# Performance work log

Hardware: AMD Instinct MI355X
Metric: run time of the kernel (lower is better)

Reference implementation:

```python
import jax, jax.numpy as jnp
import numpy as np

CLIP = 5.0
LATENT, HIDDEN, INPUT, OUT = 64, 128, 128, 32


def setup_inputs() -> dict:
    key = jax.random.key(0)
    ks = jax.random.split(key, 9)
    B, T = 256, 1024
    inp = {
        "input_sequence": jax.random.normal(ks[0], (B, T, INPUT), jnp.float32),
        "A": jax.random.uniform(ks[1], (LATENT,), jnp.float32, -0.1, 0.1),
        "W1": jax.random.normal(ks[2], (LATENT, HIDDEN), jnp.float32) * (1.0 / np.sqrt(HIDDEN)),
        "W2": jax.random.normal(ks[3], (HIDDEN, LATENT), jnp.float32) * (1.0 / np.sqrt(LATENT)),
        "h1": jnp.zeros((LATENT,), jnp.float32),
        "h2": jnp.zeros((HIDDEN,), jnp.float32),
        "C": jax.random.normal(ks[4], (LATENT, INPUT), jnp.float32) * (1.0 / np.sqrt(INPUT)),
        "Wout": jax.random.normal(ks[5], (OUT, LATENT), jnp.float32) * (1.0 / np.sqrt(LATENT)),
        "bout": jnp.zeros((OUT,), jnp.float32),
    }
    return inp


def reference(input_sequence, A, W1, W2, h1, h2, C, Wout, bout):
    # Precompute input drive C @ s_t for all timesteps: [B, T, L]
    drive = jnp.einsum('bti,li->btl', input_sequence, C)
    B = input_sequence.shape[0]
    z0 = jnp.zeros((B, A.shape[0]), input_sequence.dtype)

    def step(z, u):
        # z: [B, L], u: [B, L] (C @ s_t)
        hidden = jax.nn.relu(z @ W2.T + h2)               # [B, H]
        z_next = z * A + hidden @ W1.T + h1 + u           # [B, L]
        z_next = jnp.clip(z_next, -CLIP, CLIP)
        return z_next, None

    zT, _ = jax.lax.scan(step, z0, jnp.swapaxes(drive, 0, 1))  # scan over T
    return zT @ Wout.T + bout                                   # [B, OUT]
```

## Files before the change

kernel.cpp:

```cpp
#include <hip/hip_runtime.h>
#include <hip/hip_bf16.h>

#define BATCH 256
#define TSTEPS 1024
#define NIN 128
#define NL 64
#define NH 128
#define NOUT 32

typedef __attribute__((ext_vector_type(8))) short short8;
typedef __attribute__((ext_vector_type(4))) float f32x4;

__device__ inline int pk2(float x, float y) {
    __hip_bfloat162 h = __float22bfloat162_rn(make_float2(x, y));
    union { __hip_bfloat162 h; int i; } u;
    u.h = h;
    return u.i;
}
__device__ inline short bf1(float x) {
    __hip_bfloat16 h = __float2bfloat16(x);
    union { __hip_bfloat16 h; short s; } u;
    u.h = h;
    return u.s;
}

#define WG_BARRIER() asm volatile("s_waitcnt lgkmcnt(0)\n\ts_barrier" ::: "memory")

__launch_bounds__(256, 1)
__global__ void ugemm_mfma(const float* __restrict__ input,
                           const float* __restrict__ C,
                           const float* __restrict__ h1,
                           unsigned short* __restrict__ u16) {
    const int lane = threadIdx.x & 63;
    const int wv   = threadIdx.x >> 6;
    const int c = lane & 15;
    const int q = lane >> 4;
    const long wbase = ((long)blockIdx.x * 4 + wv) * 128;

    short8 cA[4][4];
    #pragma unroll
    for (int mt = 0; mt < 4; ++mt)
        #pragma unroll
        for (int kf = 0; kf < 4; ++kf) {
            const float* p = C + (mt * 16 + c) * NIN + kf * 32 + q * 8;
            float4 r0 = *(const float4*)p;
            float4 r1 = *(const float4*)(p + 4);
            union { short8 s; int i[4]; } f;
            f.i[0] = pk2(r0.x, r0.y); f.i[1] = pk2(r0.z, r0.w);
            f.i[2] = pk2(r1.x, r1.y); f.i[3] = pk2(r1.z, r1.w);
            cA[mt][kf] = f.s;
        }
    f32x4 h1f[4];
    #pragma unroll
    for (int mt = 0; mt < 4; ++mt)
        h1f[mt] = *(const f32x4*)(h1 + mt * 16 + q * 4);

    float4 raw[8], rawn[8];
    {
        const float* sr = input + (wbase + c) * NIN;
        #pragma unroll
        for (int kf = 0; kf < 4; ++kf) {
            raw[2*kf]   = *(const float4*)(sr + kf * 32 + q * 8);
            raw[2*kf+1] = *(const float4*)(sr + kf * 32 + q * 8 + 4);
        }
    }

    for (int it = 0; it < 8; ++it) {
        if (it < 7) {
            const float* sr = input + (wbase + (it + 1) * 16 + c) * NIN;
            #pragma unroll
            for (int kf = 0; kf < 4; ++kf) {
                rawn[2*kf]   = *(const float4*)(sr + kf * 32 + q * 8);
                rawn[2*kf+1] = *(const float4*)(sr + kf * 32 + q * 8 + 4);
            }
        }
        short8 bf[4];
        #pragma unroll
        for (int kf = 0; kf < 4; ++kf) {
            union { short8 s; int i[4]; } f;
            f.i[0] = pk2(raw[2*kf].x,   raw[2*kf].y);
            f.i[1] = pk2(raw[2*kf].z,   raw[2*kf].w);
            f.i[2] = pk2(raw[2*kf+1].x, raw[2*kf+1].y);
            f.i[3] = pk2(raw[2*kf+1].z, raw[2*kf+1].w);
            bf[kf] = f.s;
        }
        long rr = wbase + it * 16 + c;
        int b = (int)(rr >> 10), t = (int)(rr & 1023);
        unsigned short* ubase = u16 + ((size_t)t * 256 + b) * 64 + q * 4;
        #pragma unroll
        for (int mt = 0; mt < 4; ++mt) {
            f32x4 acc = __builtin_amdgcn_mfma_f32_16x16x32_bf16(cA[mt][0], bf[0], h1f[mt], 0, 0, 0);
            acc = __builtin_amdgcn_mfma_f32_16x16x32_bf16(cA[mt][1], bf[1], acc, 0, 0, 0);
            acc = __builtin_amdgcn_mfma_f32_16x16x32_bf16(cA[mt][2], bf[2], acc, 0, 0, 0);
            acc = __builtin_amdgcn_mfma_f32_16x16x32_bf16(cA[mt][3], bf[3], acc, 0, 0, 0);
            *(int2*)(ubase + mt * 16) =
                make_int2(pk2(acc[0], acc[1]), pk2(acc[2], acc[3]));
        }
        #pragma unroll
        for (int j = 0; j < 8; ++j) raw[j] = rawn[j];
    }
}

__launch_bounds__(256, 1)
__global__ void plrnn_scan_mfma(const float* __restrict__ A,
                                const float* __restrict__ W1,
                                const float* __restrict__ W2,
                                const float* __restrict__ h2,
                                const unsigned short* __restrict__ u16,
                                const float* __restrict__ Wout,
                                const float* __restrict__ bout,
                                float* __restrict__ out) {
    __shared__ __attribute__((aligned(16))) unsigned short zbuf[16 * 72];
    __shared__ __attribute__((aligned(16))) unsigned short hbuf[16 * 136];

    const int lane = threadIdx.x & 63;
    const int w    = threadIdx.x >> 6;
    const int c = lane & 15;
    const int q = lane >> 4;
    const int bbase = blockIdx.x * 16;

    short8 aw2[2][2];
    #pragma unroll
    for (int i = 0; i < 2; ++i)
        #pragma unroll
        for (int kt = 0; kt < 2; ++kt) {
            const float* p = W2 + ((2*w + i) * 16 + c) * NL + kt * 32 + q * 8;
            short8 f;
            #pragma unroll
            for (int j = 0; j < 8; ++j) f[j] = bf1(p[j]);
            aw2[i][kt] = f;
        }
    short8 aw1[4];
    #pragma unroll
    for (int kt = 0; kt < 4; ++kt) {
        const float* p = W1 + (w * 16 + c) * NH + kt * 32 + q * 8;
        short8 f;
        #pragma unroll
        for (int j = 0; j < 8; ++j) f[j] = bf1(p[j]);
        aw1[kt] = f;
    }
    f32x4 h2f[2];
    #pragma unroll
    for (int i = 0; i < 2; ++i)
        h2f[i] = *(const f32x4*)(h2 + (2*w + i) * 16 + q * 4);
    const f32x4 af = *(const f32x4*)(A + w * 16 + q * 4);

    f32x4 zf = {0.f, 0.f, 0.f, 0.f};

    const unsigned short* ub = u16 + ((size_t)(bbase + c)) * 64 + w * 16 + q * 4;
    int2 ucur = *(const int2*)ub;
    int2 unx  = *(const int2*)(ub + 16384);

    for (int t = 0; t < TSTEPS; ++t) {
        *(int2*)&zbuf[c * 72 + w * 16 + q * 4] =
            make_int2(pk2(zf[0], zf[1]), pk2(zf[2], zf[3]));
        WG_BARRIER();
        short8 bz0 = *(short8*)&zbuf[c * 72 + q * 8];
        short8 bz1 = *(short8*)&zbuf[c * 72 + 32 + q * 8];

        int tp = (t + 2 < TSTEPS) ? t + 2 : TSTEPS - 1;
        int2 upf = *(const int2*)(ub + (size_t)tp * 16384);

        #pragma unroll
        for (int i = 0; i < 2; ++i) {
            f32x4 acc = __builtin_amdgcn_mfma_f32_16x16x32_bf16(aw2[i][0], bz0, h2f[i], 0, 0, 0);
            acc = __builtin_amdgcn_mfma_f32_16x16x32_bf16(aw2[i][1], bz1, acc, 0, 0, 0);
            *(int2*)&hbuf[c * 136 + (2*w + i) * 16 + q * 4] =
                make_int2(pk2(fmaxf(acc[0], 0.f), fmaxf(acc[1], 0.f)),
                          pk2(fmaxf(acc[2], 0.f), fmaxf(acc[3], 0.f)));
        }
        WG_BARRIER();
        short8 bh0 = *(short8*)&hbuf[c * 136 + q * 8];
        short8 bh1 = *(short8*)&hbuf[c * 136 + 32 + q * 8];
        short8 bh2 = *(short8*)&hbuf[c * 136 + 64 + q * 8];
        short8 bh3 = *(short8*)&hbuf[c * 136 + 96 + q * 8];

        f32x4 cin;
        cin[0] = fmaf(zf[0], af[0], __int_as_float(ucur.x << 16));
        cin[1] = fmaf(zf[1], af[1], __int_as_float(ucur.x & 0xffff0000));
        cin[2] = fmaf(zf[2], af[2], __int_as_float(ucur.y << 16));
        cin[3] = fmaf(zf[3], af[3], __int_as_float(ucur.y & 0xffff0000));
        f32x4 acc = __builtin_amdgcn_mfma_f32_16x16x32_bf16(aw1[0], bh0, cin, 0, 0, 0);
        acc = __builtin_amdgcn_mfma_f32_16x16x32_bf16(aw1[1], bh1, acc, 0, 0, 0);
        acc = __builtin_amdgcn_mfma_f32_16x16x32_bf16(aw1[2], bh2, acc, 0, 0, 0);
        acc = __builtin_amdgcn_mfma_f32_16x16x32_bf16(aw1[3], bh3, acc, 0, 0, 0);
        #pragma unroll
        for (int e = 0; e < 4; ++e)
            zf[e] = fminf(fmaxf(acc[e], -5.f), 5.f);
        ucur = unx;
        unx  = upf;
    }

    *(int2*)&zbuf[c * 72 + w * 16 + q * 4] =
        make_int2(pk2(zf[0], zf[1]), pk2(zf[2], zf[3]));
    WG_BARRIER();
    if (w < 2) {
        short8 fz0 = *(short8*)&zbuf[c * 72 + q * 8];
        short8 fz1 = *(short8*)&zbuf[c * 72 + 32 + q * 8];
        const float* p0 = Wout + (w * 16 + c) * NL + q * 8;
        const float* p1 = p0 + 32;
        short8 fa, fb;
        #pragma unroll
        for (int j = 0; j < 8; ++j) { fa[j] = bf1(p0[j]); fb[j] = bf1(p1[j]); }
        f32x4 cb = *(const f32x4*)(bout + w * 16 + q * 4);
        f32x4 acc = __builtin_amdgcn_mfma_f32_16x16x32_bf16(fa, fz0, cb, 0, 0, 0);
        acc = __builtin_amdgcn_mfma_f32_16x16x32_bf16(fb, fz1, acc, 0, 0, 0);
        *(f32x4*)&out[(bbase + c) * 32 + w * 16 + q * 4] = acc;
    }
}

extern "C" void kernel_launch(void* const* d_in, const int* in_sizes, int n_in,
                              void* d_out, int out_size, void* d_ws, size_t ws_size,
                              hipStream_t stream) {
    const float* input = (const float*)d_in[0];
    const float* A     = (const float*)d_in[1];
    const float* W1    = (const float*)d_in[2];
    const float* W2    = (const float*)d_in[3];
    const float* h1    = (const float*)d_in[4];
    const float* h2    = (const float*)d_in[5];
    const float* C     = (const float*)d_in[6];
    const float* Wout  = (const float*)d_in[7];
    const float* bout  = (const float*)d_in[8];
    float* out = (float*)d_out;

    unsigned short* u16 = (unsigned short*)d_ws;

    ugemm_mfma<<<dim3(512), dim3(256), 0, stream>>>(input, C, h1, u16);
    plrnn_scan_mfma<<<dim3(16), dim3(256), 0, stream>>>(
        A, W1, W2, h2, u16, Wout, bout, out);
}
```

Measured before the change: 517.8 us.

## Run recurrent scan in a single wavefront per batch tile, removing barriers

The scan kernel is restructured so one 64-lane wavefront per 16-batch tile does all the per-step matmuls, instead of four waves that synchronised twice per timestep with workgroup barriers. LDS exchanges now rely only on a compiler fence because a single wave runs in lockstep. The time loop is also unrolled by two with ping-pong prefetch buffers, and clamping uses fmed3. Each wave now issues four times as many serially dependent MFMAs per step and holds more weights in registers, trading barrier latency for longer per-wave compute chains.

```diff
diff --git a/kernel.cpp b/kernel.cpp
--- a/kernel.cpp
+++ b/kernel.cpp
@@ -24,7 +24,7 @@
     return u.s;
 }
 
-#define WG_BARRIER() asm volatile("s_waitcnt lgkmcnt(0)\n\ts_barrier" ::: "memory")
+#define KFENCE() asm volatile("" ::: "memory")
 
 __launch_bounds__(256, 1)
 __global__ void ugemm_mfma(const float* __restrict__ input,
@@ -101,8 +101,8 @@
     }
 }
 
-__launch_bounds__(256, 1)
-__global__ void plrnn_scan_mfma(const float* __restrict__ A,
+__launch_bounds__(64, 1)
+__global__ void plrnn_scan_wave(const float* __restrict__ A,
                                 const float* __restrict__ W1,
                                 const float* __restrict__ W2,
                                 const float* __restrict__ h2,
@@ -110,102 +110,167 @@
                                 const float* __restrict__ Wout,
                                 const float* __restrict__ bout,
                                 float* __restrict__ out) {
-    __shared__ __attribute__((aligned(16))) unsigned short zbuf[16 * 72];
-    __shared__ __attribute__((aligned(16))) unsigned short hbuf[16 * 136];
+    __shared__ __attribute__((aligned(16))) unsigned short zs[16 * 72];
+    __shared__ __attribute__((aligned(16))) unsigned short hs[16 * 136];
 
     const int lane = threadIdx.x & 63;
-    const int w    = threadIdx.x >> 6;
     const int c = lane & 15;
     const int q = lane >> 4;
     const int bbase = blockIdx.x * 16;
 
-    short8 aw2[2][2];
-    #pragma unroll
-    for (int i = 0; i < 2; ++i)
+    short8 aw2[8][2];
+    #pragma unroll
+    for (int mt = 0; mt < 8; ++mt)
         #pragma unroll
         for (int kt = 0; kt < 2; ++kt) {
-            const float* p = W2 + ((2*w + i) * 16 + c) * NL + kt * 32 + q * 8;
+            const float* p = W2 + (mt * 16 + c) * NL + kt * 32 + q * 8;
             short8 f;
             #pragma unroll
             for (int j = 0; j < 8; ++j) f[j] = bf1(p[j]);
-            aw2[i][kt] = f;
-        }
-    short8 aw1[4];
-    #pragma unroll
-    for (int kt = 0; kt < 4; ++kt) {
-        const float* p = W1 + (w * 16 + c) * NH + kt * 32 + q * 8;
-        short8 f;
-        #pragma unroll
-        for (int j = 0; j < 8; ++j) f[j] = bf1(p[j]);
-        aw1[kt] = f;
-    }
-    f32x4 h2f[2];
-    #pragma unroll
-    for (int i = 0; i < 2; ++i)
-        h2f[i] = *(const f32x4*)(h2 + (2*w + i) * 16 + q * 4);
-    const f32x4 af = *(const f32x4*)(A + w * 16 + q * 4);
-
-    f32x4 zf = {0.f, 0.f, 0.f, 0.f};
-
-    const unsigned short* ub = u16 + ((size_t)(bbase + c)) * 64 + w * 16 + q * 4;
-    int2 ucur = *(const int2*)ub;
-    int2 unx  = *(const int2*)(ub + 16384);
-
-    for (int t = 0; t < TSTEPS; ++t) {
-        *(int2*)&zbuf[c * 72 + w * 16 + q * 4] =
-            make_int2(pk2(zf[0], zf[1]), pk2(zf[2], zf[3]));
-        WG_BARRIER();
-        short8 bz0 = *(short8*)&zbuf[c * 72 + q * 8];
-        short8 bz1 = *(short8*)&zbuf[c * 72 + 32 + q * 8];
-
-        int tp = (t + 2 < TSTEPS) ? t + 2 : TSTEPS - 1;
-        int2 upf = *(const int2*)(ub + (size_t)tp * 16384);
-
-        #pragma unroll
-        for (int i = 0; i < 2; ++i) {
-            f32x4 acc = __builtin_amdgcn_mfma_f32_16x16x32_bf16(aw2[i][0], bz0, h2f[i], 0, 0, 0);
-            acc = __builtin_amdgcn_mfma_f32_16x16x32_bf16(aw2[i][1], bz1, acc, 0, 0, 0);
-            *(int2*)&hbuf[c * 136 + (2*w + i) * 16 + q * 4] =
-                make_int2(pk2(fmaxf(acc[0], 0.f), fmaxf(acc[1], 0.f)),
-                          pk2(fmaxf(acc[2], 0.f), fmaxf(acc[3], 0.f)));
-        }
-        WG_BARRIER();
-        short8 bh0 = *(short8*)&hbuf[c * 136 + q * 8];
-        short8 bh1 = *(short8*)&hbuf[c * 136 + 32 + q * 8];
-        short8 bh2 = *(short8*)&hbuf[c * 136 + 64 + q * 8];
-        short8 bh3 = *(short8*)&hbuf[c * 136 + 96 + q * 8];
-
-        f32x4 cin;
-        cin[0] = fmaf(zf[0], af[0], __int_as_float(ucur.x << 16));
-        cin[1] = fmaf(zf[1], af[1], __int_as_float(ucur.x & 0xffff0000));
-        cin[2] = fmaf(zf[2], af[2], __int_as_float(ucur.y << 16));
-        cin[3] = fmaf(zf[3], af[3], __int_as_float(ucur.y & 0xffff0000));
-        f32x4 acc = __builtin_amdgcn_mfma_f32_16x16x32_bf16(aw1[0], bh0, cin, 0, 0, 0);
-        acc = __builtin_amdgcn_mfma_f32_16x16x32_bf16(aw1[1], bh1, acc, 0, 0, 0);
-        acc = __builtin_amdgcn_mfma_f32_16x16x32_bf16(aw1[2], bh2, acc, 0, 0, 0);
-        acc = __builtin_amdgcn_mfma_f32_16x16x32_bf16(aw1[3], bh3, acc, 0, 0, 0);
-        #pragma unroll
-        for (int e = 0; e < 4; ++e)
-            zf[e] = fminf(fmaxf(acc[e], -5.f), 5.f);
-        ucur = unx;
-        unx  = upf;
-    }
-
-    *(int2*)&zbuf[c * 72 + w * 16 + q * 4] =
-        make_int2(pk2(zf[0], zf[1]), pk2(zf[2], zf[3]));
-    WG_BARRIER();
-    if (w < 2) {
-        short8 fz0 = *(short8*)&zbuf[c * 72 + q * 8];
-        short8 fz1 = *(short8*)&zbuf[c * 72 + 32 + q * 8];
-        const float* p0 = Wout + (w * 16 + c) * NL + q * 8;
-        const float* p1 = p0 + 32;
-        short8 fa, fb;
-        #pragma unroll
-        for (int j = 0; j < 8; ++j) { fa[j] = bf1(p0[j]); fb[j] = bf1(p1[j]); }
-        f32x4 cb = *(const f32x4*)(bout + w * 16 + q * 4);
-        f32x4 acc = __builtin_amdgcn_mfma_f32_16x16x32_bf16(fa, fz0, cb, 0, 0, 0);
-        acc = __builtin_amdgcn_mfma_f32_16x16x32_bf16(fb, fz1, acc, 0, 0, 0);
-        *(f32x4*)&out[(bbase + c) * 32 + w * 16 + q * 4] = acc;
+            aw2[mt][kt] = f;
+        }
+    short8 aw1[4][4];
+    #pragma unroll
+    for (int lt = 0; lt < 4; ++lt)
+        #pragma unroll
+        for (int kt = 0; kt < 4; ++kt) {
+            const float* p = W1 + (lt * 16 + c) * NH + kt * 32 + q * 8;
+            short8 f;
+            #pragma unroll
+            for (int j = 0; j < 8; ++j) f[j] = bf1(p[j]);
+            aw1[lt][kt] = f;
+        }
+    f32x4 h2f[8];
+    #pragma unroll
+    for (int mt = 0; mt < 8; ++mt)
+        h2f[mt] = *(const f32x4*)(h2 + mt * 16 + q * 4);
+    f32x4 af[4];
+    #pragma unroll
+    for (int lt = 0; lt < 4; ++lt)
+        af[lt] = *(const f32x4*)(A + lt * 16 + q * 4);
+
+    const unsigned short* ub = u16 + (size_t)(bbase + c) * 64 + q * 4;
+    int2 uP[4], uQ[4];
+    #pragma unroll
+    for (int lt = 0; lt < 4; ++lt) {
+        uP[lt] = *(const int2*)(ub + lt * 16);
+        uQ[lt] = *(const int2*)(ub + 16384 + lt * 16);
+    }
+
+    f32x4 zf[4];
+    #pragma unroll
+    for (int lt = 0; lt < 4; ++lt) zf[lt] = (f32x4){0.f, 0.f, 0.f, 0.f};
+
+    short8 bz0 = (short8){0, 0, 0, 0, 0, 0, 0, 0};
+    short8 bz1 = (short8){0, 0, 0, 0, 0, 0, 0, 0};
+
+    f32x4 cin[4];
+    #pragma unroll
+    for (int lt = 0; lt < 4; ++lt) {
+        cin[lt][0] = __int_as_float(uP[lt].x << 16);
+        cin[lt][1] = __int_as_float(uP[lt].x & 0xffff0000);
+        cin[lt][2] = __int_as_float(uP[lt].y << 16);
+        cin[lt][3] = __int_as_float(uP[lt].y & 0xffff0000);
+    }
+
+    auto step = [&](int2 (&pf)[4], const int2 (&tail)[4], const int T) {
+        f32x4 ha[4];
+        #pragma unroll
+        for (int mt = 0; mt < 4; ++mt)
+            ha[mt] = __builtin_amdgcn_mfma_f32_16x16x32_bf16(aw2[mt][0], bz0, h2f[mt], 0, 0, 0);
+        #pragma unroll
+        for (int mt = 0; mt < 4; ++mt)
+            ha[mt] = __builtin_amdgcn_mfma_f32_16x16x32_bf16(aw2[mt][1], bz1, ha[mt], 0, 0, 0);
+        #pragma unroll
+        for (int mt = 0; mt < 4; ++mt)
+            *(int2*)&hs[c * 136 + mt * 16 + q * 4] = make_int2(
+                pk2(fmaxf(ha[mt][0], 0.f), fmaxf(ha[mt][1], 0.f)),
+                pk2(fmaxf(ha[mt][2], 0.f), fmaxf(ha[mt][3], 0.f)));
+        KFENCE();
+        short8 bh0 = *(short8*)&hs[c * 136 + q * 8];
+        short8 bh1 = *(short8*)&hs[c * 136 + 32 + q * 8];
+
+        f32x4 hb[4];
+        #pragma unroll
+        for (int mt = 0; mt < 4; ++mt)
+            hb[mt] = __builtin_amdgcn_mfma_f32_16x16x32_bf16(aw2[mt + 4][0], bz0, h2f[mt + 4], 0, 0, 0);
+        #pragma unroll
+        for (int mt = 0; mt < 4; ++mt)
+            hb[mt] = __builtin_amdgcn_mfma_f32_16x16x32_bf16(aw2[mt + 4][1], bz1, hb[mt], 0, 0, 0);
+        #pragma unroll
+        for (int mt = 0; mt < 4; ++mt)
+            *(int2*)&hs[c * 136 + (mt + 4) * 16 + q * 4] = make_int2(
+                pk2(fmaxf(hb[mt][0], 0.f), fmaxf(hb[mt][1], 0.f)),
+                pk2(fmaxf(hb[mt][2], 0.f), fmaxf(hb[mt][3], 0.f)));
+        KFENCE();
+        short8 bh2 = *(short8*)&hs[c * 136 + 64 + q * 8];
+        short8 bh3 = *(short8*)&hs[c * 136 + 96 + q * 8];
+
+        const int tp = (T + 2 < TSTEPS) ? T + 2 : TSTEPS - 1;
+        #pragma unroll
+        for (int lt = 0; lt < 4; ++lt)
+            pf[lt] = *(const int2*)(ub + (size_t)tp * 16384 + lt * 16);
+
+        f32x4 za[4];
+        #pragma unroll
+        for (int lt = 0; lt < 4; ++lt)
+            za[lt] = __builtin_amdgcn_mfma_f32_16x16x32_bf16(aw1[lt][0], bh0, cin[lt], 0, 0, 0);
+        #pragma unroll
+        for (int lt = 0; lt < 4; ++lt)
+            za[lt] = __builtin_amdgcn_mfma_f32_16x16x32_bf16(aw1[lt][1], bh1, za[lt], 0, 0, 0);
+        #pragma unroll
+        for (int lt = 0; lt < 4; ++lt)
+            za[lt] = __builtin_amdgcn_mfma_f32_16x16x32_bf16(aw1[lt][2], bh2, za[lt], 0, 0, 0);
+        #pragma unroll
+        for (int lt = 0; lt < 4; ++lt)
+            za[lt] = __builtin_amdgcn_mfma_f32_16x16x32_bf16(aw1[lt][3], bh3, za[lt], 0, 0, 0);
+
+        #pragma unroll
+        for (int lt = 0; lt < 4; ++lt) {
+            zf[lt][0] = __builtin_amdgcn_fmed3f(za[lt][0], -5.f, 5.f);
+            zf[lt][1] = __builtin_amdgcn_fmed3f(za[lt][1], -5.f, 5.f);
+            zf[lt][2] = __builtin_amdgcn_fmed3f(za[lt][2], -5.f, 5.f);
+            zf[lt][3] = __builtin_amdgcn_fmed3f(za[lt][3], -5.f, 5.f);
+        }
+        #pragma unroll
+        for (int lt = 0; lt < 4; ++lt)
+            *(int2*)&zs[c * 72 + lt * 16 + q * 4] =
+                make_int2(pk2(zf[lt][0], zf[lt][1]), pk2(zf[lt][2], zf[lt][3]));
+        KFENCE();
+        bz0 = *(short8*)&zs[c * 72 + q * 8];
+        bz1 = *(short8*)&zs[c * 72 + 32 + q * 8];
+
+        #pragma unroll
+        for (int lt = 0; lt < 4; ++lt) {
+            cin[lt][0] = fmaf(zf[lt][0], af[lt][0], __int_as_float(tail[lt].x << 16));
+            cin[lt][1] = fmaf(zf[lt][1], af[lt][1], __int_as_float(tail[lt].x & 0xffff0000));
+            cin[lt][2] = fmaf(zf[lt][2], af[lt][2], __int_as_float(tail[lt].y << 16));
+            cin[lt][3] = fmaf(zf[lt][3], af[lt][3], __int_as_float(tail[lt].y & 0xffff0000));
+        }
+    };
+
+    for (int t = 0; t < TSTEPS; t += 2) {
+        step(uP, uQ, t);
+        step(uQ, uP, t + 1);
+    }
+
+    short8 wo[2][2];
+    #pragma unroll
+    for (int ot = 0; ot < 2; ++ot)
+        #pragma unroll
+        for (int kt = 0; kt < 2; ++kt) {
+            const float* p = Wout + (ot * 16 + c) * NL + kt * 32 + q * 8;
+            short8 f;
+            #pragma unroll
+            for (int j = 0; j < 8; ++j) f[j] = bf1(p[j]);
+            wo[ot][kt] = f;
+        }
+    #pragma unroll
+    for (int ot = 0; ot < 2; ++ot) {
+        f32x4 ob = *(const f32x4*)(bout + ot * 16 + q * 4);
+        f32x4 acc = __builtin_amdgcn_mfma_f32_16x16x32_bf16(wo[ot][0], bz0, ob, 0, 0, 0);
+        acc = __builtin_amdgcn_mfma_f32_16x16x32_bf16(wo[ot][1], bz1, acc, 0, 0, 0);
+        *(f32x4*)&out[(size_t)(bbase + c) * 32 + ot * 16 + q * 4] = acc;
     }
 }
 
@@ -226,6 +291,6 @@
     unsigned short* u16 = (unsigned short*)d_ws;
 
     ugemm_mfma<<<dim3(512), dim3(256), 0, stream>>>(input, C, h1, u16);
-    plrnn_scan_mfma<<<dim3(16), dim3(256), 0, stream>>>(
+    plrnn_scan_wave<<<dim3(16), dim3(64), 0, stream>>>(
         A, W1, W2, h2, u16, Wout, bout, out);
 }
```

Result: slower. 835.7 us (+61.4%).

## Split-K the W1 GEMM across waves and rebuild fragments with permlane swaps

Applied to the files above, without the earlier changes.

The recurrent scan kernel now has each wave own a K-slice of the hidden dimension for the W1 product. Each wave computes partial sums for all latent tiles, and the partials are reduced through a double-buffered LDS buffer. The B fragments for h and z are built in registers with permlane32/permlane16 swaps instead of round-tripping through LDS. This drops one workgroup barrier per timestep, trading it for extra MFMAs, more LDS traffic for the partials, and redundant reduction work in every wave.

```diff
diff --git a/kernel.cpp b/kernel.cpp
--- a/kernel.cpp
+++ b/kernel.cpp
@@ -10,6 +10,7 @@
 
 typedef __attribute__((ext_vector_type(8))) short short8;
 typedef __attribute__((ext_vector_type(4))) float f32x4;
+typedef __attribute__((ext_vector_type(2))) unsigned int u32x2;
 
 __device__ inline int pk2(float x, float y) {
     __hip_bfloat162 h = __float22bfloat162_rn(make_float2(x, y));
@@ -25,6 +26,19 @@
 }
 
 #define WG_BARRIER() asm volatile("s_waitcnt lgkmcnt(0)\n\ts_barrier" ::: "memory")
+
+__device__ inline short8 mk_bfrag(int a0, int a1, int b0, int b1) {
+    u32x2 s0 = __builtin_amdgcn_permlane32_swap((unsigned)a0, (unsigned)b0, false, false);
+    u32x2 t0 = __builtin_amdgcn_permlane16_swap(s0[0], s0[1], false, false);
+    u32x2 s1 = __builtin_amdgcn_permlane32_swap((unsigned)a1, (unsigned)b1, false, false);
+    u32x2 t1 = __builtin_amdgcn_permlane16_swap(s1[0], s1[1], false, false);
+    union { int i[4]; short8 s; } u;
+    u.i[0] = (int)t0[0];
+    u.i[1] = (int)t1[0];
+    u.i[2] = (int)t0[1];
+    u.i[3] = (int)t1[1];
+    return u.s;
+}
 
 __launch_bounds__(256, 1)
 __global__ void ugemm_mfma(const float* __restrict__ input,
@@ -102,16 +116,15 @@
 }
 
 __launch_bounds__(256, 1)
-__global__ void plrnn_scan_mfma(const float* __restrict__ A,
-                                const float* __restrict__ W1,
-                                const float* __restrict__ W2,
-                                const float* __restrict__ h2,
-                                const unsigned short* __restrict__ u16,
-                                const float* __restrict__ Wout,
-                                const float* __restrict__ bout,
-                                float* __restrict__ out) {
-    __shared__ __attribute__((aligned(16))) unsigned short zbuf[16 * 72];
-    __shared__ __attribute__((aligned(16))) unsigned short hbuf[16 * 136];
+__global__ void plrnn_scan_ks(const float* __restrict__ A,
+                              const float* __restrict__ W1,
+                              const float* __restrict__ W2,
+                              const float* __restrict__ h2,
+                              const unsigned short* __restrict__ u16,
+                              const float* __restrict__ Wout,
+                              const float* __restrict__ bout,
+                              float* __restrict__ out) {
+    __shared__ __attribute__((aligned(16))) float pbuf[2][4][4][64][4];
 
     const int lane = threadIdx.x & 63;
     const int w    = threadIdx.x >> 6;
@@ -124,7 +137,7 @@
     for (int i = 0; i < 2; ++i)
         #pragma unroll
         for (int kt = 0; kt < 2; ++kt) {
-            const float* p = W2 + ((2*w + i) * 16 + c) * NL + kt * 32 + q * 8;
+            const float* p = W2 + ((2 * w + i) * 16 + c) * NL + kt * 32 + q * 8;
             short8 f;
             #pragma unroll
             for (int j = 0; j < 8; ++j) f[j] = bf1(p[j]);
@@ -132,80 +145,116 @@
         }
     short8 aw1[4];
     #pragma unroll
-    for (int kt = 0; kt < 4; ++kt) {
-        const float* p = W1 + (w * 16 + c) * NH + kt * 32 + q * 8;
+    for (int lt = 0; lt < 4; ++lt) {
+        const float* p = W1 + (lt * 16 + c) * NH + w * 32 + q * 8;
         short8 f;
         #pragma unroll
         for (int j = 0; j < 8; ++j) f[j] = bf1(p[j]);
-        aw1[kt] = f;
+        aw1[lt] = f;
     }
     f32x4 h2f[2];
     #pragma unroll
     for (int i = 0; i < 2; ++i)
-        h2f[i] = *(const f32x4*)(h2 + (2*w + i) * 16 + q * 4);
+        h2f[i] = *(const f32x4*)(h2 + (2 * w + i) * 16 + q * 4);
     const f32x4 af = *(const f32x4*)(A + w * 16 + q * 4);
 
-    f32x4 zf = {0.f, 0.f, 0.f, 0.f};
-
-    const unsigned short* ub = u16 + ((size_t)(bbase + c)) * 64 + w * 16 + q * 4;
-    int2 ucur = *(const int2*)ub;
-    int2 unx  = *(const int2*)(ub + 16384);
-
-    for (int t = 0; t < TSTEPS; ++t) {
-        *(int2*)&zbuf[c * 72 + w * 16 + q * 4] =
-            make_int2(pk2(zf[0], zf[1]), pk2(zf[2], zf[3]));
+    const unsigned short* ub = u16 + (size_t)(bbase + c) * 64 + w * 16 + q * 4;
+    int2 uP = *(const int2*)ub;
+    int2 uQ = *(const int2*)(ub + 16384);
+
+    short8 bz0 = (short8){0, 0, 0, 0, 0, 0, 0, 0};
+    short8 bz1 = (short8){0, 0, 0, 0, 0, 0, 0, 0};
+    f32x4 cin;
+    cin[0] = __int_as_float(uP.x << 16);
+    cin[1] = __int_as_float(uP.x & 0xffff0000);
+    cin[2] = __int_as_float(uP.y << 16);
+    cin[3] = __int_as_float(uP.y & 0xffff0000);
+    const f32x4 zero4 = {0.f, 0.f, 0.f, 0.f};
+
+    auto step = [&](int2& pf, const int2& tail, const int T, const int buf) {
+        f32x4 ha[2];
+        #pragma unroll
+        for (int i = 0; i < 2; ++i)
+            ha[i] = __builtin_amdgcn_mfma_f32_16x16x32_bf16(aw2[i][0], bz0, h2f[i], 0, 0, 0);
+        #pragma unroll
+        for (int i = 0; i < 2; ++i)
+            ha[i] = __builtin_amdgcn_mfma_f32_16x16x32_bf16(aw2[i][1], bz1, ha[i], 0, 0, 0);
+
+        int hp[2][2];
+        #pragma unroll
+        for (int i = 0; i < 2; ++i) {
+            hp[i][0] = pk2(fmaxf(ha[i][0], 0.f), fmaxf(ha[i][1], 0.f));
+            hp[i][1] = pk2(fmaxf(ha[i][2], 0.f), fmaxf(ha[i][3], 0.f));
+        }
+        short8 bh = mk_bfrag(hp[0][0], hp[0][1], hp[1][0], hp[1][1]);
+
+        f32x4 za[4];
+        #pragma unroll
+        for (int lt = 0; lt < 4; ++lt)
+            za[lt] = __builtin_amdgcn_mfma_f32_16x16x32_bf16(
+                aw1[lt], bh, (lt == w) ? cin : zero4, 0, 0, 0);
+
+        #pragma unroll
+        for (int lt = 0; lt < 4; ++lt)
+            *(f32x4*)&pbuf[buf][w][lt][lane][0] = za[lt];
+
         WG_BARRIER();
-        short8 bz0 = *(short8*)&zbuf[c * 72 + q * 8];
-        short8 bz1 = *(short8*)&zbuf[c * 72 + 32 + q * 8];
-
-        int tp = (t + 2 < TSTEPS) ? t + 2 : TSTEPS - 1;
-        int2 upf = *(const int2*)(ub + (size_t)tp * 16384);
-
-        #pragma unroll
-        for (int i = 0; i < 2; ++i) {
-            f32x4 acc = __builtin_amdgcn_mfma_f32_16x16x32_bf16(aw2[i][0], bz0, h2f[i], 0, 0, 0);
-            acc = __builtin_amdgcn_mfma_f32_16x16x32_bf16(aw2[i][1], bz1, acc, 0, 0, 0);
-            *(int2*)&hbuf[c * 136 + (2*w + i) * 16 + q * 4] =
-                make_int2(pk2(fmaxf(acc[0], 0.f), fmaxf(acc[1], 0.f)),
-                          pk2(fmaxf(acc[2], 0.f), fmaxf(acc[3], 0.f)));
-        }
-        WG_BARRIER();
-        short8 bh0 = *(short8*)&hbuf[c * 136 + q * 8];
-        short8 bh1 = *(short8*)&hbuf[c * 136 + 32 + q * 8];
-        short8 bh2 = *(short8*)&hbuf[c * 136 + 64 + q * 8];
-        short8 bh3 = *(short8*)&hbuf[c * 136 + 96 + q * 8];
-
-        f32x4 cin;
-        cin[0] = fmaf(zf[0], af[0], __int_as_float(ucur.x << 16));
-        cin[1] = fmaf(zf[1], af[1], __int_as_float(ucur.x & 0xffff0000));
-        cin[2] = fmaf(zf[2], af[2], __int_as_float(ucur.y << 16));
-        cin[3] = fmaf(zf[3], af[3], __int_as_float(ucur.y & 0xffff0000));
-        f32x4 acc = __builtin_amdgcn_mfma_f32_16x16x32_bf16(aw1[0], bh0, cin, 0, 0, 0);
-        acc = __builtin_amdgcn_mfma_f32_16x16x32_bf16(aw1[1], bh1, acc, 0, 0, 0);
-        acc = __builtin_amdgcn_mfma_f32_16x16x32_bf16(aw1[2], bh2, acc, 0, 0, 0);
-        acc = __builtin_amdgcn_mfma_f32_16x16x32_bf16(aw1[3], bh3, acc, 0, 0, 0);
-        #pragma unroll
-        for (int e = 0; e < 4; ++e)
-            zf[e] = fminf(fmaxf(acc[e], -5.f), 5.f);
-        ucur = unx;
-        unx  = upf;
-    }
-
-    *(int2*)&zbuf[c * 72 + w * 16 + q * 4] =
-        make_int2(pk2(zf[0], zf[1]), pk2(zf[2], zf[3]));
-    WG_BARRIER();
+
+        const int tp = (T + 2 < TSTEPS) ? T + 2 : TSTEPS - 1;
+        pf = *(const int2*)(ub + (size_t)tp * 16384);
+
+        #pragma unroll
+        for (int d = 1; d < 4; ++d) {
+            const int v = (w + d) & 3;
+            #pragma unroll
+            for (int lt = 0; lt < 4; ++lt) {
+                f32x4 p = *(const f32x4*)&pbuf[buf][v][lt][lane][0];
+                za[lt][0] += p[0]; za[lt][1] += p[1];
+                za[lt][2] += p[2]; za[lt][3] += p[3];
+            }
+        }
+
+        int zp[4][2];
+        f32x4 zw;
+        #pragma unroll
+        for (int lt = 0; lt < 4; ++lt) {
+            f32x4 zc;
+            zc[0] = __builtin_amdgcn_fmed3f(za[lt][0], -5.f, 5.f);
+            zc[1] = __builtin_amdgcn_fmed3f(za[lt][1], -5.f, 5.f);
+            zc[2] = __builtin_amdgcn_fmed3f(za[lt][2], -5.f, 5.f);
+            zc[3] = __builtin_amdgcn_fmed3f(za[lt][3], -5.f, 5.f);
+            zp[lt][0] = pk2(zc[0], zc[1]);
+            zp[lt][1] = pk2(zc[2], zc[3]);
+            if (lt == w) zw = zc;
+        }
+        bz0 = mk_bfrag(zp[0][0], zp[0][1], zp[1][0], zp[1][1]);
+        bz1 = mk_bfrag(zp[2][0], zp[2][1], zp[3][0], zp[3][1]);
+
+        cin[0] = fmaf(zw[0], af[0], __int_as_float(tail.x << 16));
+        cin[1] = fmaf(zw[1], af[1], __int_as_float(tail.x & 0xffff0000));
+        cin[2] = fmaf(zw[2], af[2], __int_as_float(tail.y << 16));
+        cin[3] = fmaf(zw[3], af[3], __int_as_float(tail.y & 0xffff0000));
+    };
+
+    for (int t = 0; t < TSTEPS; t += 2) {
+        step(uP, uQ, t, 0);
+        step(uQ, uP, t + 1, 1);
+    }
+
     if (w < 2) {
-        short8 fz0 = *(short8*)&zbuf[c * 72 + q * 8];
-        short8 fz1 = *(short8*)&zbuf[c * 72 + 32 + q * 8];
-        const float* p0 = Wout + (w * 16 + c) * NL + q * 8;
-        const float* p1 = p0 + 32;
-        short8 fa, fb;
-        #pragma unroll
-        for (int j = 0; j < 8; ++j) { fa[j] = bf1(p0[j]); fb[j] = bf1(p1[j]); }
-        f32x4 cb = *(const f32x4*)(bout + w * 16 + q * 4);
-        f32x4 acc = __builtin_amdgcn_mfma_f32_16x16x32_bf16(fa, fz0, cb, 0, 0, 0);
-        acc = __builtin_amdgcn_mfma_f32_16x16x32_bf16(fb, fz1, acc, 0, 0, 0);
-        *(f32x4*)&out[(bbase + c) * 32 + w * 16 + q * 4] = acc;
+        short8 wo[2];
+        #pragma unroll
+        for (int kt = 0; kt < 2; ++kt) {
+            const float* p = Wout + (w * 16 + c) * NL + kt * 32 + q * 8;
+            short8 f;
+            #pragma unroll
+            for (int j = 0; j < 8; ++j) f[j] = bf1(p[j]);
+            wo[kt] = f;
+        }
+        f32x4 ob = *(const f32x4*)(bout + w * 16 + q * 4);
+        f32x4 acc = __builtin_amdgcn_mfma_f32_16x16x32_bf16(wo[0], bz0, ob, 0, 0, 0);
+        acc = __builtin_amdgcn_mfma_f32_16x16x32_bf16(wo[1], bz1, acc, 0, 0, 0);
+        *(f32x4*)&out[(size_t)(bbase + c) * 32 + w * 16 + q * 4] = acc;
     }
 }
 
@@ -226,6 +275,6 @@
     unsigned short* u16 = (unsigned short*)d_ws;
 
     ugemm_mfma<<<dim3(512), dim3(256), 0, stream>>>(input, C, h1, u16);
-    plrnn_scan_mfma<<<dim3(16), dim3(256), 0, stream>>>(
+    plrnn_scan_ks<<<dim3(16), dim3(256), 0, stream>>>(
         A, W1, W2, h2, u16, Wout, bout, out);
 }
```

After: 843.5 us. +62.9%, slower.
